# Optimization experiments

Measured on AMD Instinct MI355X. Metric: run time of the kernel, lower is better.

The kernel has to match this reference:

```python
import jax, jax.numpy as jnp
import numpy as np

B, N, D, H = 16, 512, 256, 8
DK = D // H
EPS = 1e-6
NEG_INF = 1e12
LAM_ATT, LAM_DIST, LAM_ADJ = 0.3, 0.3, 0.4


def setup_inputs() -> dict:
    key = jax.random.key(0)
    ks = jax.random.split(key, 16)
    inp = {
        "query": jax.random.normal(ks[0], (B, N, D), jnp.float32),
        "key": jax.random.normal(ks[1], (B, N, D), jnp.float32),
        "value": jax.random.normal(ks[2], (B, N, D), jnp.float32),
        "adj_matrix": jax.random.uniform(ks[3], (B, N, N), jnp.float32),
        "distances_matrix": jax.random.uniform(ks[4], (B, N, N), jnp.float32),
        "edges_att": jnp.zeros((1,), jnp.float32),
        "mask": jnp.ones((B, N), jnp.int32),
    }
    s = 1.0 / np.sqrt(D)
    # four Linear(d_model, d_model): Wq, Wk, Wv, Wo (+ biases)
    for i, nm in enumerate(["q", "k", "v", "o"]):
        inp[f"W{nm}"] = jax.random.normal(ks[5 + 2 * i], (D, D), jnp.float32) * s
        inp[f"b{nm}"] = jax.random.normal(ks[6 + 2 * i], (D,), jnp.float32) * s
    return inp


def _proj(x, W, b):
    # [B,N,D] -> [B,H,N,DK]
    y = x @ W.T + b
    return y.reshape(B, N, H, DK).transpose(0, 2, 1, 3)


def reference(query, key, value, adj_matrix, distances_matrix, edges_att, mask,
              Wq, bq, Wk, bk, Wv, bv, Wo, bo):
    q = _proj(query, Wq, bq)
    k = _proj(key, Wk, bk)
    v = _proj(value, Wv, bv)

    valid = mask != 0  # [B,N] key-side validity

    # distance kernel: softmax(-d) over keys, masked positions -> 0 prob
    d_scores = jnp.where(valid[:, None, :], -distances_matrix, -jnp.inf)
    p_dist = jax.nn.softmax(d_scores, axis=-1)  # [B,N,N]

    # scaled dot-product attention with key mask
    scores = jnp.einsum("bhqd,bhkd->bhqk", q, k) / np.sqrt(DK)
    scores = jnp.where(valid[:, None, None, :], scores, -NEG_INF)
    p_attn = jax.nn.softmax(scores, axis=-1)  # [B,H,N,N]

    # row-normalized adjacency
    p_adj = adj_matrix / (adj_matrix.sum(axis=-1, keepdims=True) + EPS)  # [B,N,N]

    # blend three attention terms (broadcast dist/adj over heads)
    p_weighted = (LAM_ATT * p_attn
                  + LAM_DIST * p_dist[:, None]
                  + LAM_ADJ * p_adj[:, None])  # [B,H,N,N]

    x = jnp.einsum("bhqk,bhkd->bhqd", p_weighted, v)  # [B,H,N,DK]
    x = x.transpose(0, 2, 1, 3).reshape(B, N, D)
    out = x @ Wo.T + bo  # output projection (4th linear)
    return out
```

## Files before the change

kernel.cpp:

```cpp
#include <hip/hip_runtime.h>
#include <cstdint>
#include <cstddef>

#define B_  16
#define N_  512
#define D_  256
#define H_  8
#define DK_ 32

#define QKV_ELEMS 2097152

__device__ __align__(16) unsigned short g_Qb[QKV_ELEMS];
__device__ __align__(16) unsigned short g_Kb[QKV_ELEMS];
__device__ __align__(16) unsigned short g_VT[QKV_ELEMS];
__device__ __align__(16) unsigned short g_WqB[D_*D_];
__device__ __align__(16) unsigned short g_WkB[D_*D_];
__device__ __align__(16) unsigned short g_WvB[D_*D_];
__device__ __align__(16) unsigned short g_WoB[D_*D_];
__device__ __align__(16) unsigned short g_ST[B_*N_*N_];

typedef short v8s __attribute__((ext_vector_type(8)));
typedef float v4f __attribute__((ext_vector_type(4)));

__device__ __forceinline__ unsigned short f2b(float f){
  unsigned int x;
  __builtin_memcpy(&x, &f, 4);
  x = x + 0x7FFFu + ((x >> 16) & 1u);
  return (unsigned short)(x >> 16);
}
__device__ __forceinline__ v8s pack8(const float4 a, const float4 b){
  v8s o;
  o[0]=(short)f2b(a.x); o[1]=(short)f2b(a.y); o[2]=(short)f2b(a.z); o[3]=(short)f2b(a.w);
  o[4]=(short)f2b(b.x); o[5]=(short)f2b(b.y); o[6]=(short)f2b(b.z); o[7]=(short)f2b(b.w);
  return o;
}

__global__ __launch_bounds__(256) void prep_w(
    const float* __restrict__ Wq, const float* __restrict__ Wk,
    const float* __restrict__ Wv, const float* __restrict__ Wo)
{
  const int bid = blockIdx.x;
  const int z = bid >> 6;
  const int i = ((bid & 63)*256 + (int)threadIdx.x)*4;
  const float* src = (z==0)?Wq:(z==1)?Wk:(z==2)?Wv:Wo;
  const float4 u = *reinterpret_cast<const float4*>(src + i);
  ushort4 o4;
  o4.x = f2b(u.x); o4.y = f2b(u.y); o4.z = f2b(u.z); o4.w = f2b(u.w);
  if (z < 3){
    unsigned short* dst = (z==0)?g_WqB:(z==1)?g_WkB:g_WvB;
    *reinterpret_cast<ushort4*>(dst + i) = o4;
  } else {
    const int n = i >> 8, k = i & 255;
    *reinterpret_cast<ushort4*>(g_WoB + ((size_t)(k >> 5))*8192 + (size_t)n*32 + (k & 31)) = o4;
  }
}

__global__ __launch_bounds__(512) void st_kernel(
    const float* __restrict__ dist, const float* __restrict__ adjm,
    const int* __restrict__ mask)
{
  const int bid = blockIdx.x;
  const int b = bid & 15, qt = bid >> 4, q0 = qt*16;
  const int t = threadIdx.x;
  const int row = t >> 5, seg = t & 31;
  const size_t roff = ((size_t)(b*N_ + q0 + row))*N_ + seg*16;
  const float* dp = dist + roff;
  const float* ap = adjm + roff;
  const int*   mp = mask + b*N_ + seg*16;
  const float4 d0 = reinterpret_cast<const float4*>(dp)[0];
  const float4 d1 = reinterpret_cast<const float4*>(dp)[1];
  const float4 d2 = reinterpret_cast<const float4*>(dp)[2];
  const float4 d3 = reinterpret_cast<const float4*>(dp)[3];
  const float4 a0 = reinterpret_cast<const float4*>(ap)[0];
  const float4 a1 = reinterpret_cast<const float4*>(ap)[1];
  const float4 a2 = reinterpret_cast<const float4*>(ap)[2];
  const float4 a3 = reinterpret_cast<const float4*>(ap)[3];
  const int4   m0 = reinterpret_cast<const int4*>(mp)[0];
  const int4   m1 = reinterpret_cast<const int4*>(mp)[1];
  const int4   m2 = reinterpret_cast<const int4*>(mp)[2];
  const int4   m3 = reinterpret_cast<const int4*>(mp)[3];

  float ev[16], av[16];
  #define ST_STEP(i, d4, a4, m4) \
    ev[i+0] = m4.x ? __expf(-d4.x) : 0.f;  av[i+0] = a4.x; \
    ev[i+1] = m4.y ? __expf(-d4.y) : 0.f;  av[i+1] = a4.y; \
    ev[i+2] = m4.z ? __expf(-d4.z) : 0.f;  av[i+2] = a4.z; \
    ev[i+3] = m4.w ? __expf(-d4.w) : 0.f;  av[i+3] = a4.w;
  ST_STEP(0,  d0, a0, m0)
  ST_STEP(4,  d1, a1, m1)
  ST_STEP(8,  d2, a2, m2)
  ST_STEP(12, d3, a3, m3)
  #undef ST_STEP
  float lz = 0.f, la = 0.f;
  #pragma unroll
  for (int i = 0; i < 16; ++i){ lz += ev[i]; la += av[i]; }
  #pragma unroll
  for (int o = 1; o < 32; o <<= 1){
    lz += __shfl_xor(lz, o, 64);
    la += __shfl_xor(la, o, 64);
  }
  const float c0 = (lz > 0.f) ? 0.3f / lz : 0.f;
  const float c1 = 0.4f / (la + 1e-6f);
  v8s s0, s1;
  #pragma unroll
  for (int i = 0; i < 8; ++i){
    s0[i] = (short)f2b(ev[i]*c0   + av[i]*c1);
    s1[i] = (short)f2b(ev[8+i]*c0 + av[8+i]*c1);
  }
  *reinterpret_cast<v8s*>(g_ST + roff)     = s0;
  *reinterpret_cast<v8s*>(g_ST + roff + 8) = s1;
}

__global__ __launch_bounds__(256) void qkv_gemm(
    const float* __restrict__ query, const float* __restrict__ key_,
    const float* __restrict__ value,
    const float* __restrict__ bq, const float* __restrict__ bk,
    const float* __restrict__ bv)
{
  __shared__ unsigned short Wl[64*264];
  const int bid = blockIdx.x;
  const int t   = threadIdx.x;
  const int z  = bid >> 9;
  const int rr = bid & 511;
  const int mt = rr >> 2, nt = rr & 3;
  const float* Ap = (z==0) ? query : (z==1) ? key_ : value;
  const unsigned short* WB = (z==0) ? g_WqB : (z==1) ? g_WkB : g_WvB;
  const float* bp = (z==0) ? bq : (z==1) ? bk : bv;
  const int w = t >> 6, lane = t & 63, kl = lane & 15, quad = lane >> 4;
  const int m0 = mt*64 + w*16;
  const int n0 = nt*64;

  {
    const int row = t >> 2;
    const int ks  = (t & 3) * 64;
    const unsigned short* src = WB + (size_t)(n0+row)*256 + ks;
    unsigned short* dst = Wl + row*264 + ks;
    #pragma unroll
    for (int u = 0; u < 8; ++u)
      *reinterpret_cast<v8s*>(dst + u*8) = *reinterpret_cast<const v8s*>(src + u*8);
  }
  __syncthreads();

  v4f acc[4];
  #pragma unroll
  for (int nb = 0; nb < 4; ++nb) acc[nb] = (v4f){0.f,0.f,0.f,0.f};
  const int arow = m0 + kl;

  if (z == 2){
    #pragma unroll
    for (int k0 = 0; k0 < 256; k0 += 32){
      const float* ap = Ap + (size_t)arow*256 + k0 + quad*8;
      const v8s af = pack8(reinterpret_cast<const float4*>(ap)[0],
                           reinterpret_cast<const float4*>(ap)[1]);
      #pragma unroll
      for (int nb = 0; nb < 4; ++nb){
        const v8s wf = *reinterpret_cast<const v8s*>(&Wl[(nb*16+kl)*264 + k0 + quad*8]);
        acc[nb] = __builtin_amdgcn_mfma_f32_16x16x32_bf16(wf, af, acc[nb], 0, 0, 0);
      }
    }
    const int tok = m0 + kl, bb = tok >> 9, nr = tok & 511;
    #pragma unroll
    for (int nb = 0; nb < 4; ++nb)
      #pragma unroll
      for (int r = 0; r < 4; ++r){
        const int n = n0 + nb*16 + quad*4 + r;
        const float v = acc[nb][r] + bp[n];
        g_VT[(((size_t)bb*H_ + (n>>5))*16 + (nr>>5))*1024 + (size_t)(n&31)*32 + (nr&31)] = f2b(v);
      }
  } else {
    #pragma unroll
    for (int k0 = 0; k0 < 256; k0 += 32){
      const float* ap = Ap + (size_t)arow*256 + k0 + quad*8;
      const v8s af = pack8(reinterpret_cast<const float4*>(ap)[0],
                           reinterpret_cast<const float4*>(ap)[1]);
      #pragma unroll
      for (int nb = 0; nb < 4; ++nb){
        const v8s wf = *reinterpret_cast<const v8s*>(&Wl[(nb*16+kl)*264 + k0 + quad*8]);
        acc[nb] = __builtin_amdgcn_mfma_f32_16x16x32_bf16(af, wf, acc[nb], 0, 0, 0);
      }
    }
    unsigned short* dst = z ? g_Kb : g_Qb;
    #pragma unroll
    for (int nb = 0; nb < 4; ++nb){
      const int n = n0 + nb*16 + kl;
      const float bias = bp[n];
      #pragma unroll
      for (int r = 0; r < 4; ++r){
        const int m = m0 + quad*4 + r;
        const float v = acc[nb][r] + bias;
        dst[(((size_t)(m>>9)*H_ + (n>>5))*N_ + (m&511))*DK_ + (n&31)] = f2b(v);
      }
    }
  }
}

__global__ __launch_bounds__(512, 4) void attn_kernel(
    const int* __restrict__ mask, const float* __restrict__ bo,
    float* __restrict__ out)
{
  __shared__ unsigned short STl[16*520];
  __shared__ unsigned short Pl[8*16*40];
  __shared__ unsigned short Xl[16*272];
  const int bid = blockIdx.x;
  const int b  = bid & 15;
  const int qt = bid >> 4;
  const int q0 = qt*16;
  const int t  = threadIdx.x;
  const int w  = t >> 6, lane = t & 63;
  const int kl = lane & 15, quad = lane >> 4;

  {
    const int row = t >> 5;
    const int c16 = (t & 31) * 16;
    const unsigned short* src = g_ST + ((size_t)(b*N_ + q0 + row))*N_ + c16;
    *reinterpret_cast<v8s*>(&STl[row*520 + c16])     = *reinterpret_cast<const v8s*>(src);
    *reinterpret_cast<v8s*>(&STl[row*520 + c16 + 8]) = *reinterpret_cast<const v8s*>(src + 8);
  }

  const int h = w;
  const size_t bh = (size_t)b*H_ + h;
  const float scale = 0.17677669529663687f;
  const unsigned short* Qp = g_Qb + (bh*N_ + q0)*DK_;
  const unsigned short* Kp = g_Kb + bh*N_*DK_;
  const unsigned short* Vp = g_VT + bh*(size_t)(N_*DK_);
  unsigned short* Plw = Pl + w*640;
  const int* mrow = mask + b*N_;
  const v8s aq = *reinterpret_cast<const v8s*>(Qp + (size_t)kl*DK_ + quad*8);
  const v4f vz = {0.f, 0.f, 0.f, 0.f};

  v4f oA0 = vz, oA1 = vz;
  v4f oS0 = vz, oS1 = vz;
  float lsum[4] = {0.f, 0.f, 0.f, 0.f};

  __syncthreads();

  #pragma unroll 1
  for (int ch = 0; ch < 4; ++ch){
    const int k0 = ch*128;
    v4f acc[8];
    #pragma unroll
    for (int kb = 0; kb < 8; ++kb){
      const v8s bk = *reinterpret_cast<const v8s*>(Kp + (size_t)(k0 + kb*16 + kl)*DK_ + quad*8);
      acc[kb] = __builtin_amdgcn_mfma_f32_16x16x32_bf16(aq, bk, vz, 0, 0, 0);
    }
    #pragma unroll
    for (int kb = 0; kb < 8; ++kb){
      const bool valid = (mrow[k0 + kb*16 + kl] != 0);
      #pragma unroll
      for (int r = 0; r < 4; ++r){
        const float e = valid ? __expf(acc[kb][r]*scale) : 0.f;
        acc[kb][r] = e;
        lsum[r] += e;
      }
    }
    #pragma unroll
    for (int cc = 0; cc < 4; ++cc){
      #pragma unroll
      for (int r = 0; r < 4; ++r){
        Plw[(quad*4 + r)*40 + kl]      = f2b(acc[2*cc    ][r]);
        Plw[(quad*4 + r)*40 + 16 + kl] = f2b(acc[2*cc + 1][r]);
      }
      const int kk = k0 + cc*32;
      const v8s bp  = *reinterpret_cast<const v8s*>(&Plw[kl*40 + quad*8]);
      const v8s bst = *reinterpret_cast<const v8s*>(&STl[kl*520 + kk + quad*8]);
      const v8s av0 = *reinterpret_cast<const v8s*>(Vp + (size_t)(kk + kl)*32 + quad*8);
      const v8s av1 = *reinterpret_cast<const v8s*>(Vp + (size_t)(kk + 16 + kl)*32 + quad*8);
      oA0 = __builtin_amdgcn_mfma_f32_16x16x32_bf16(av0, bp,  oA0, 0, 0, 0);
      oS0 = __builtin_amdgcn_mfma_f32_16x16x32_bf16(av0, bst, oS0, 0, 0, 0);
      oA1 = __builtin_amdgcn_mfma_f32_16x16x32_bf16(av1, bp,  oA1, 0, 0, 0);
      oS1 = __builtin_amdgcn_mfma_f32_16x16x32_bf16(av1, bst, oS1, 0, 0, 0);
    }
  }

  #pragma unroll
  for (int r = 0; r < 4; ++r)
    #pragma unroll
    for (int o = 1; o < 16; o <<= 1) lsum[r] += __shfl_xor(lsum[r], o, 64);
  const float s01 = (kl & 1) ? lsum[1] : lsum[0];
  const float s23 = (kl & 1) ? lsum[3] : lsum[2];
  const float sv  = (kl & 2) ? s23 : s01;
  float inv = __shfl(sv, ((kl >> 2) << 4) | (kl & 3), 64);
  inv = (inv > 0.f) ? 0.3f / inv : 0.f;

  unsigned short* xr = Xl + kl*272 + h*32;
  #pragma unroll
  for (int r = 0; r < 4; ++r){
    xr[     quad*4 + r] = f2b(oA0[r]*inv + oS0[r]);
    xr[16 + quad*4 + r] = f2b(oA1[r]*inv + oS1[r]);
  }
  __syncthreads();

  {
    const int n0 = w*32;
    v4f a2[2];
    a2[0] = vz; a2[1] = vz;
    #pragma unroll
    for (int k0 = 0; k0 < 256; k0 += 32){
      const v8s af = *reinterpret_cast<const v8s*>(&Xl[kl*272 + k0 + quad*8]);
      #pragma unroll
      for (int nb = 0; nb < 2; ++nb){
        const v8s wf = *reinterpret_cast<const v8s*>(
            g_WoB + (size_t)(k0 >> 5)*8192 + (size_t)(n0 + nb*16 + kl)*32 + quad*8);
        a2[nb] = __builtin_amdgcn_mfma_f32_16x16x32_bf16(af, wf, a2[nb], 0, 0, 0);
      }
    }
    #pragma unroll
    for (int nb = 0; nb < 2; ++nb){
      const int n = n0 + nb*16 + kl;
      const float bias = bo[n];
      #pragma unroll
      for (int r = 0; r < 4; ++r)
        out[((size_t)(b*N_ + q0 + quad*4 + r))*256 + n] = a2[nb][r] + bias;
    }
  }
}

extern "C" void kernel_launch(void* const* d_in, const int* in_sizes, int n_in,
                              void* d_out, int out_size, void* d_ws, size_t ws_size,
                              hipStream_t stream)
{
  const float* query = (const float*)d_in[0];
  const float* key_  = (const float*)d_in[1];
  const float* value = (const float*)d_in[2];
  const float* adjm  = (const float*)d_in[3];
  const float* dist  = (const float*)d_in[4];
  const int*   mask  = (const int*)d_in[6];
  const float* Wq = (const float*)d_in[7];  const float* bq = (const float*)d_in[8];
  const float* Wk = (const float*)d_in[9];  const float* bk = (const float*)d_in[10];
  const float* Wv = (const float*)d_in[11]; const float* bv = (const float*)d_in[12];
  const float* Wo = (const float*)d_in[13]; const float* bo = (const float*)d_in[14];

  prep_w<<<256, 256, 0, stream>>>(Wq, Wk, Wv, Wo);
  st_kernel<<<512, 512, 0, stream>>>(dist, adjm, mask);
  qkv_gemm<<<1536, 256, 0, stream>>>(query, key_, value, bq, bk, bv);
  attn_kernel<<<512, 512, 0, stream>>>(mask, bo, (float*)d_out);
}
```

Measured before the change: 165.0 us.

## Merge weight prep into ST kernel and prefetch V/mask before softmax in attention

Weight conversion to bf16 now runs in 32 extra blocks of the ST kernel, removing one launch. In the attention loop, V fragments and mask values for the whole 128-key chunk are loaded up front so their latency overlaps the exp work. All probabilities for the chunk are then written to a wider shared buffer in one pass instead of being interleaved with the PV MFMAs. This raises register and LDS use per block (Pl goes from about 10KB to 35KB), which may cut occupancy below the 4 blocks per CU requested.

```diff
diff --git a/kernel.cpp b/kernel.cpp
--- a/kernel.cpp
+++ b/kernel.cpp
@@ -35,33 +35,39 @@
   return o;
 }
 
-__global__ __launch_bounds__(256) void prep_w(
+__global__ __launch_bounds__(512) void st_prep(
+    const float* __restrict__ dist, const float* __restrict__ adjm,
+    const int* __restrict__ mask,
     const float* __restrict__ Wq, const float* __restrict__ Wk,
     const float* __restrict__ Wv, const float* __restrict__ Wo)
 {
   const int bid = blockIdx.x;
-  const int z = bid >> 6;
-  const int i = ((bid & 63)*256 + (int)threadIdx.x)*4;
-  const float* src = (z==0)?Wq:(z==1)?Wk:(z==2)?Wv:Wo;
-  const float4 u = *reinterpret_cast<const float4*>(src + i);
-  ushort4 o4;
-  o4.x = f2b(u.x); o4.y = f2b(u.y); o4.z = f2b(u.z); o4.w = f2b(u.w);
-  if (z < 3){
-    unsigned short* dst = (z==0)?g_WqB:(z==1)?g_WkB:g_WvB;
-    *reinterpret_cast<ushort4*>(dst + i) = o4;
-  } else {
-    const int n = i >> 8, k = i & 255;
-    *reinterpret_cast<ushort4*>(g_WoB + ((size_t)(k >> 5))*8192 + (size_t)n*32 + (k & 31)) = o4;
-  }
-}
-
-__global__ __launch_bounds__(512) void st_kernel(
-    const float* __restrict__ dist, const float* __restrict__ adjm,
-    const int* __restrict__ mask)
-{
-  const int bid = blockIdx.x;
+  const int t = threadIdx.x;
+
+  if (bid >= 512){
+    const int tid = (bid - 512)*512 + t;
+    #pragma unroll
+    for (int u = 0; u < 4; ++u){
+      const int i4 = tid*4 + u;
+      const int i  = i4*4;
+      const int z  = i >> 16;
+      const int lo = i & 65535;
+      const float* src = (z==0)?Wq:(z==1)?Wk:(z==2)?Wv:Wo;
+      const float4 f = *reinterpret_cast<const float4*>(src + lo);
+      ushort4 o4;
+      o4.x=f2b(f.x); o4.y=f2b(f.y); o4.z=f2b(f.z); o4.w=f2b(f.w);
+      if (z < 3){
+        unsigned short* dst = (z==0)?g_WqB:(z==1)?g_WkB:g_WvB;
+        *reinterpret_cast<ushort4*>(dst + lo) = o4;
+      } else {
+        const int n = lo >> 8, k = lo & 255;
+        *reinterpret_cast<ushort4*>(g_WoB + ((size_t)(k >> 5))*8192 + (size_t)n*32 + (k & 31)) = o4;
+      }
+    }
+    return;
+  }
+
   const int b = bid & 15, qt = bid >> 4, q0 = qt*16;
-  const int t = threadIdx.x;
   const int row = t >> 5, seg = t & 31;
   const size_t roff = ((size_t)(b*N_ + q0 + row))*N_ + seg*16;
   const float* dp = dist + roff;
@@ -199,7 +205,7 @@
     float* __restrict__ out)
 {
   __shared__ unsigned short STl[16*520];
-  __shared__ unsigned short Pl[8*16*40];
+  __shared__ unsigned short Pl[8*16*136];
   __shared__ unsigned short Xl[16*272];
   const int bid = blockIdx.x;
   const int b  = bid & 15;
@@ -223,7 +229,7 @@
   const unsigned short* Qp = g_Qb + (bh*N_ + q0)*DK_;
   const unsigned short* Kp = g_Kb + bh*N_*DK_;
   const unsigned short* Vp = g_VT + bh*(size_t)(N_*DK_);
-  unsigned short* Plw = Pl + w*640;
+  unsigned short* Plw = Pl + w*2176;
   const int* mrow = mask + b*N_;
   const v8s aq = *reinterpret_cast<const v8s*>(Qp + (size_t)kl*DK_ + quad*8);
   const v4f vz = {0.f, 0.f, 0.f, 0.f};
@@ -243,9 +249,19 @@
       const v8s bk = *reinterpret_cast<const v8s*>(Kp + (size_t)(k0 + kb*16 + kl)*DK_ + quad*8);
       acc[kb] = __builtin_amdgcn_mfma_f32_16x16x32_bf16(aq, bk, vz, 0, 0, 0);
     }
+    v8s av[8];
+    int mk[8];
+    #pragma unroll
+    for (int cc = 0; cc < 4; ++cc){
+      const int kk = k0 + cc*32;
+      av[2*cc]   = *reinterpret_cast<const v8s*>(Vp + (size_t)(kk + kl)*32 + quad*8);
+      av[2*cc+1] = *reinterpret_cast<const v8s*>(Vp + (size_t)(kk + 16 + kl)*32 + quad*8);
+    }
+    #pragma unroll
+    for (int kb = 0; kb < 8; ++kb) mk[kb] = mrow[k0 + kb*16 + kl];
     #pragma unroll
     for (int kb = 0; kb < 8; ++kb){
-      const bool valid = (mrow[k0 + kb*16 + kl] != 0);
+      const bool valid = (mk[kb] != 0);
       #pragma unroll
       for (int r = 0; r < 4; ++r){
         const float e = valid ? __expf(acc[kb][r]*scale) : 0.f;
@@ -254,21 +270,19 @@
       }
     }
     #pragma unroll
+    for (int kb = 0; kb < 8; ++kb)
+      #pragma unroll
+      for (int r = 0; r < 4; ++r)
+        Plw[(quad*4 + r)*136 + kb*16 + kl] = f2b(acc[kb][r]);
+    #pragma unroll
     for (int cc = 0; cc < 4; ++cc){
-      #pragma unroll
-      for (int r = 0; r < 4; ++r){
-        Plw[(quad*4 + r)*40 + kl]      = f2b(acc[2*cc    ][r]);
-        Plw[(quad*4 + r)*40 + 16 + kl] = f2b(acc[2*cc + 1][r]);
-      }
       const int kk = k0 + cc*32;
-      const v8s bp  = *reinterpret_cast<const v8s*>(&Plw[kl*40 + quad*8]);
+      const v8s bp  = *reinterpret_cast<const v8s*>(&Plw[kl*136 + cc*32 + quad*8]);
       const v8s bst = *reinterpret_cast<const v8s*>(&STl[kl*520 + kk + quad*8]);
-      const v8s av0 = *reinterpret_cast<const v8s*>(Vp + (size_t)(kk + kl)*32 + quad*8);
-      const v8s av1 = *reinterpret_cast<const v8s*>(Vp + (size_t)(kk + 16 + kl)*32 + quad*8);
-      oA0 = __builtin_amdgcn_mfma_f32_16x16x32_bf16(av0, bp,  oA0, 0, 0, 0);
-      oS0 = __builtin_amdgcn_mfma_f32_16x16x32_bf16(av0, bst, oS0, 0, 0, 0);
-      oA1 = __builtin_amdgcn_mfma_f32_16x16x32_bf16(av1, bp,  oA1, 0, 0, 0);
-      oS1 = __builtin_amdgcn_mfma_f32_16x16x32_bf16(av1, bst, oS1, 0, 0, 0);
+      oA0 = __builtin_amdgcn_mfma_f32_16x16x32_bf16(av[2*cc],   bp,  oA0, 0, 0, 0);
+      oS0 = __builtin_amdgcn_mfma_f32_16x16x32_bf16(av[2*cc],   bst, oS0, 0, 0, 0);
+      oA1 = __builtin_amdgcn_mfma_f32_16x16x32_bf16(av[2*cc+1], bp,  oA1, 0, 0, 0);
+      oS1 = __builtin_amdgcn_mfma_f32_16x16x32_bf16(av[2*cc+1], bst, oS1, 0, 0, 0);
     }
   }
 
@@ -330,8 +344,7 @@
   const float* Wv = (const float*)d_in[11]; const float* bv = (const float*)d_in[12];
   const float* Wo = (const float*)d_in[13]; const float* bo = (const float*)d_in[14];
 
-  prep_w<<<256, 256, 0, stream>>>(Wq, Wk, Wv, Wo);
-  st_kernel<<<512, 512, 0, stream>>>(dist, adjm, mask);
+  st_prep<<<544, 512, 0, stream>>>(dist, adjm, mask, Wq, Wk, Wv, Wo);
   qkv_gemm<<<1536, 256, 0, stream>>>(query, key_, value, bq, bk, bv);
   attn_kernel<<<512, 512, 0, stream>>>(mask, bo, (float*)d_out);
 }
```

Result: no change. 163.7 us (-0.8%).

## Merge ST prep into QKV GEMM launch and keep attention probabilities in registers

Applied to the files above, without the earlier changes.

Combines the distance/adjacency blend kernel with the QKV projection into one launch, with extra blocks handling ST rows, and remaps block indices for the GEMM part. Folds the softmax scale and log2(e) into Q so attention can use exp2 directly. Swaps the MFMA operand order so the scores come out transposed, then passes P to the PV MFMA through packed bf16 converts and cross-lane shuffles instead of an LDS round trip. It also simplifies the row-sum reduction. This removes one launch, the LDS traffic for P and per-element scale multiplies, at the cost of more shuffles and a more fragile lane mapping.

```diff
diff --git a/kernel.cpp b/kernel.cpp
--- a/kernel.cpp
+++ b/kernel.cpp
@@ -21,6 +21,8 @@
 
 typedef short v8s __attribute__((ext_vector_type(8)));
 typedef float v4f __attribute__((ext_vector_type(4)));
+
+#define QSCALE 0.25503485917270874f
 
 __device__ __forceinline__ unsigned short f2b(float f){
   unsigned int x;
@@ -55,71 +57,73 @@
   }
 }
 
-__global__ __launch_bounds__(512) void st_kernel(
+__global__ __launch_bounds__(256) void st_gemm(
+    const float* __restrict__ query, const float* __restrict__ key_,
+    const float* __restrict__ value,
+    const float* __restrict__ bq, const float* __restrict__ bk,
+    const float* __restrict__ bv,
     const float* __restrict__ dist, const float* __restrict__ adjm,
     const int* __restrict__ mask)
 {
-  const int bid = blockIdx.x;
-  const int b = bid & 15, qt = bid >> 4, q0 = qt*16;
-  const int t = threadIdx.x;
-  const int row = t >> 5, seg = t & 31;
-  const size_t roff = ((size_t)(b*N_ + q0 + row))*N_ + seg*16;
-  const float* dp = dist + roff;
-  const float* ap = adjm + roff;
-  const int*   mp = mask + b*N_ + seg*16;
-  const float4 d0 = reinterpret_cast<const float4*>(dp)[0];
-  const float4 d1 = reinterpret_cast<const float4*>(dp)[1];
-  const float4 d2 = reinterpret_cast<const float4*>(dp)[2];
-  const float4 d3 = reinterpret_cast<const float4*>(dp)[3];
-  const float4 a0 = reinterpret_cast<const float4*>(ap)[0];
-  const float4 a1 = reinterpret_cast<const float4*>(ap)[1];
-  const float4 a2 = reinterpret_cast<const float4*>(ap)[2];
-  const float4 a3 = reinterpret_cast<const float4*>(ap)[3];
-  const int4   m0 = reinterpret_cast<const int4*>(mp)[0];
-  const int4   m1 = reinterpret_cast<const int4*>(mp)[1];
-  const int4   m2 = reinterpret_cast<const int4*>(mp)[2];
-  const int4   m3 = reinterpret_cast<const int4*>(mp)[3];
-
-  float ev[16], av[16];
-  #define ST_STEP(i, d4, a4, m4) \
-    ev[i+0] = m4.x ? __expf(-d4.x) : 0.f;  av[i+0] = a4.x; \
-    ev[i+1] = m4.y ? __expf(-d4.y) : 0.f;  av[i+1] = a4.y; \
-    ev[i+2] = m4.z ? __expf(-d4.z) : 0.f;  av[i+2] = a4.z; \
-    ev[i+3] = m4.w ? __expf(-d4.w) : 0.f;  av[i+3] = a4.w;
-  ST_STEP(0,  d0, a0, m0)
-  ST_STEP(4,  d1, a1, m1)
-  ST_STEP(8,  d2, a2, m2)
-  ST_STEP(12, d3, a3, m3)
-  #undef ST_STEP
-  float lz = 0.f, la = 0.f;
-  #pragma unroll
-  for (int i = 0; i < 16; ++i){ lz += ev[i]; la += av[i]; }
-  #pragma unroll
-  for (int o = 1; o < 32; o <<= 1){
-    lz += __shfl_xor(lz, o, 64);
-    la += __shfl_xor(la, o, 64);
-  }
-  const float c0 = (lz > 0.f) ? 0.3f / lz : 0.f;
-  const float c1 = 0.4f / (la + 1e-6f);
-  v8s s0, s1;
-  #pragma unroll
-  for (int i = 0; i < 8; ++i){
-    s0[i] = (short)f2b(ev[i]*c0   + av[i]*c1);
-    s1[i] = (short)f2b(ev[8+i]*c0 + av[8+i]*c1);
-  }
-  *reinterpret_cast<v8s*>(g_ST + roff)     = s0;
-  *reinterpret_cast<v8s*>(g_ST + roff + 8) = s1;
-}
-
-__global__ __launch_bounds__(256) void qkv_gemm(
-    const float* __restrict__ query, const float* __restrict__ key_,
-    const float* __restrict__ value,
-    const float* __restrict__ bq, const float* __restrict__ bk,
-    const float* __restrict__ bv)
-{
   __shared__ unsigned short Wl[64*264];
-  const int bid = blockIdx.x;
-  const int t   = threadIdx.x;
+  const int bid0 = blockIdx.x;
+  const int t    = threadIdx.x;
+
+  if (bid0 >= 1536){
+    const int s = bid0 - 1536;
+    const int b = (s >> 1) & 15, qt = s >> 5, half = s & 1;
+    const int row = half*8 + (t >> 5);
+    const int seg = t & 31;
+    const size_t roff = ((size_t)(b*N_ + qt*16 + row))*N_ + seg*16;
+    const float* dp = dist + roff;
+    const float* ap = adjm + roff;
+    const int*   mp = mask + b*N_ + seg*16;
+    const float4 d0 = reinterpret_cast<const float4*>(dp)[0];
+    const float4 d1 = reinterpret_cast<const float4*>(dp)[1];
+    const float4 d2 = reinterpret_cast<const float4*>(dp)[2];
+    const float4 d3 = reinterpret_cast<const float4*>(dp)[3];
+    const float4 a0 = reinterpret_cast<const float4*>(ap)[0];
+    const float4 a1 = reinterpret_cast<const float4*>(ap)[1];
+    const float4 a2 = reinterpret_cast<const float4*>(ap)[2];
+    const float4 a3 = reinterpret_cast<const float4*>(ap)[3];
+    const int4   m0 = reinterpret_cast<const int4*>(mp)[0];
+    const int4   m1 = reinterpret_cast<const int4*>(mp)[1];
+    const int4   m2 = reinterpret_cast<const int4*>(mp)[2];
+    const int4   m3 = reinterpret_cast<const int4*>(mp)[3];
+
+    float ev[16], av[16];
+    #define ST_STEP(i, d4, a4, m4) \
+      ev[i+0] = m4.x ? __expf(-d4.x) : 0.f;  av[i+0] = a4.x; \
+      ev[i+1] = m4.y ? __expf(-d4.y) : 0.f;  av[i+1] = a4.y; \
+      ev[i+2] = m4.z ? __expf(-d4.z) : 0.f;  av[i+2] = a4.z; \
+      ev[i+3] = m4.w ? __expf(-d4.w) : 0.f;  av[i+3] = a4.w;
+    ST_STEP(0,  d0, a0, m0)
+    ST_STEP(4,  d1, a1, m1)
+    ST_STEP(8,  d2, a2, m2)
+    ST_STEP(12, d3, a3, m3)
+    #undef ST_STEP
+    float lz = 0.f, la = 0.f;
+    #pragma unroll
+    for (int i = 0; i < 16; ++i){ lz += ev[i]; la += av[i]; }
+    #pragma unroll
+    for (int o = 1; o < 32; o <<= 1){
+      lz += __shfl_xor(lz, o, 64);
+      la += __shfl_xor(la, o, 64);
+    }
+    const float c0 = (lz > 0.f) ? 0.3f / lz : 0.f;
+    const float c1 = 0.4f / (la + 1e-6f);
+    v8s s0v, s1v;
+    #pragma unroll
+    for (int i = 0; i < 8; ++i){
+      s0v[i] = (short)f2b(ev[i]*c0   + av[i]*c1);
+      s1v[i] = (short)f2b(ev[8+i]*c0 + av[8+i]*c1);
+    }
+    *reinterpret_cast<v8s*>(g_ST + roff)     = s0v;
+    *reinterpret_cast<v8s*>(g_ST + roff + 8) = s1v;
+    return;
+  }
+
+  const int bid = ((bid0 & 7) * 192) + (bid0 >> 3);
   const int z  = bid >> 9;
   const int rr = bid & 511;
   const int mt = rr >> 2, nt = rr & 3;
@@ -180,6 +184,7 @@
       }
     }
     unsigned short* dst = z ? g_Kb : g_Qb;
+    const float sc = (z == 0) ? QSCALE : 1.0f;
     #pragma unroll
     for (int nb = 0; nb < 4; ++nb){
       const int n = n0 + nb*16 + kl;
@@ -187,7 +192,7 @@
       #pragma unroll
       for (int r = 0; r < 4; ++r){
         const int m = m0 + quad*4 + r;
-        const float v = acc[nb][r] + bias;
+        const float v = (acc[nb][r] + bias) * sc;
         dst[(((size_t)(m>>9)*H_ + (n>>5))*N_ + (m&511))*DK_ + (n&31)] = f2b(v);
       }
     }
@@ -199,7 +204,6 @@
     float* __restrict__ out)
 {
   __shared__ unsigned short STl[16*520];
-  __shared__ unsigned short Pl[8*16*40];
   __shared__ unsigned short Xl[16*272];
   const int bid = blockIdx.x;
   const int b  = bid & 15;
@@ -219,18 +223,20 @@
 
   const int h = w;
   const size_t bh = (size_t)b*H_ + h;
-  const float scale = 0.17677669529663687f;
   const unsigned short* Qp = g_Qb + (bh*N_ + q0)*DK_;
   const unsigned short* Kp = g_Kb + bh*N_*DK_;
   const unsigned short* Vp = g_VT + bh*(size_t)(N_*DK_);
-  unsigned short* Plw = Pl + w*640;
   const int* mrow = mask + b*N_;
   const v8s aq = *reinterpret_cast<const v8s*>(Qp + (size_t)kl*DK_ + quad*8);
   const v4f vz = {0.f, 0.f, 0.f, 0.f};
 
+  const int s0 = ((quad & 1) << 5) + kl;
+  const int s1 = s0 + 16;
+  const int hi = quad >> 1;
+
   v4f oA0 = vz, oA1 = vz;
   v4f oS0 = vz, oS1 = vz;
-  float lsum[4] = {0.f, 0.f, 0.f, 0.f};
+  float lsum = 0.f;
 
   __syncthreads();
 
@@ -241,46 +247,57 @@
     #pragma unroll
     for (int kb = 0; kb < 8; ++kb){
       const v8s bk = *reinterpret_cast<const v8s*>(Kp + (size_t)(k0 + kb*16 + kl)*DK_ + quad*8);
-      acc[kb] = __builtin_amdgcn_mfma_f32_16x16x32_bf16(aq, bk, vz, 0, 0, 0);
+      acc[kb] = __builtin_amdgcn_mfma_f32_16x16x32_bf16(bk, aq, vz, 0, 0, 0);
+    }
+    v8s av[8];
+    #pragma unroll
+    for (int cc = 0; cc < 4; ++cc){
+      const int kk = k0 + cc*32;
+      av[2*cc]   = *reinterpret_cast<const v8s*>(Vp + (size_t)(kk + kl)*32 + quad*8);
+      av[2*cc+1] = *reinterpret_cast<const v8s*>(Vp + (size_t)(kk + 16 + kl)*32 + quad*8);
     }
     #pragma unroll
     for (int kb = 0; kb < 8; ++kb){
-      const bool valid = (mrow[k0 + kb*16 + kl] != 0);
-      #pragma unroll
-      for (int r = 0; r < 4; ++r){
-        const float e = valid ? __expf(acc[kb][r]*scale) : 0.f;
-        acc[kb][r] = e;
-        lsum[r] += e;
-      }
+      const int4 m4 = *reinterpret_cast<const int4*>(mrow + k0 + kb*16 + quad*4);
+      const float e0 = m4.x ? __builtin_amdgcn_exp2f(acc[kb][0]) : 0.f;
+      const float e1 = m4.y ? __builtin_amdgcn_exp2f(acc[kb][1]) : 0.f;
+      const float e2 = m4.z ? __builtin_amdgcn_exp2f(acc[kb][2]) : 0.f;
+      const float e3 = m4.w ? __builtin_amdgcn_exp2f(acc[kb][3]) : 0.f;
+      acc[kb][0]=e0; acc[kb][1]=e1; acc[kb][2]=e2; acc[kb][3]=e3;
+      lsum += e0+e1+e2+e3;
     }
     #pragma unroll
     for (int cc = 0; cc < 4; ++cc){
-      #pragma unroll
-      for (int r = 0; r < 4; ++r){
-        Plw[(quad*4 + r)*40 + kl]      = f2b(acc[2*cc    ][r]);
-        Plw[(quad*4 + r)*40 + 16 + kl] = f2b(acc[2*cc + 1][r]);
-      }
       const int kk = k0 + cc*32;
-      const v8s bp  = *reinterpret_cast<const v8s*>(&Plw[kl*40 + quad*8]);
+      uint32_t pkE0, pkE2, pkO0, pkO2;
+      asm("v_cvt_pk_bf16_f32 %0, %1, %2" : "=v"(pkE0) : "v"(acc[2*cc][0]),   "v"(acc[2*cc][1]));
+      asm("v_cvt_pk_bf16_f32 %0, %1, %2" : "=v"(pkE2) : "v"(acc[2*cc][2]),   "v"(acc[2*cc][3]));
+      asm("v_cvt_pk_bf16_f32 %0, %1, %2" : "=v"(pkO0) : "v"(acc[2*cc+1][0]), "v"(acc[2*cc+1][1]));
+      asm("v_cvt_pk_bf16_f32 %0, %1, %2" : "=v"(pkO2) : "v"(acc[2*cc+1][2]), "v"(acc[2*cc+1][3]));
+      const uint32_t e0a = (uint32_t)__shfl((int)pkE0, s0, 64);
+      const uint32_t o0a = (uint32_t)__shfl((int)pkO0, s0, 64);
+      const uint32_t e2a = (uint32_t)__shfl((int)pkE2, s0, 64);
+      const uint32_t o2a = (uint32_t)__shfl((int)pkO2, s0, 64);
+      const uint32_t e0b = (uint32_t)__shfl((int)pkE0, s1, 64);
+      const uint32_t o0b = (uint32_t)__shfl((int)pkO0, s1, 64);
+      const uint32_t e2b = (uint32_t)__shfl((int)pkE2, s1, 64);
+      const uint32_t o2b = (uint32_t)__shfl((int)pkO2, s1, 64);
+      union { v8s v; uint32_t w4[4]; } bp;
+      bp.w4[0] = hi ? o0a : e0a;
+      bp.w4[1] = hi ? o2a : e2a;
+      bp.w4[2] = hi ? o0b : e0b;
+      bp.w4[3] = hi ? o2b : e2b;
       const v8s bst = *reinterpret_cast<const v8s*>(&STl[kl*520 + kk + quad*8]);
-      const v8s av0 = *reinterpret_cast<const v8s*>(Vp + (size_t)(kk + kl)*32 + quad*8);
-      const v8s av1 = *reinterpret_cast<const v8s*>(Vp + (size_t)(kk + 16 + kl)*32 + quad*8);
-      oA0 = __builtin_amdgcn_mfma_f32_16x16x32_bf16(av0, bp,  oA0, 0, 0, 0);
-      oS0 = __builtin_amdgcn_mfma_f32_16x16x32_bf16(av0, bst, oS0, 0, 0, 0);
-      oA1 = __builtin_amdgcn_mfma_f32_16x16x32_bf16(av1, bp,  oA1, 0, 0, 0);
-      oS1 = __builtin_amdgcn_mfma_f32_16x16x32_bf16(av1, bst, oS1, 0, 0, 0);
-    }
-  }
-
-  #pragma unroll
-  for (int r = 0; r < 4; ++r)
-    #pragma unroll
-    for (int o = 1; o < 16; o <<= 1) lsum[r] += __shfl_xor(lsum[r], o, 64);
-  const float s01 = (kl & 1) ? lsum[1] : lsum[0];
-  const float s23 = (kl & 1) ? lsum[3] : lsum[2];
-  const float sv  = (kl & 2) ? s23 : s01;
-  float inv = __shfl(sv, ((kl >> 2) << 4) | (kl & 3), 64);
-  inv = (inv > 0.f) ? 0.3f / inv : 0.f;
+      oA0 = __builtin_amdgcn_mfma_f32_16x16x32_bf16(av[2*cc],   bp.v, oA0, 0, 0, 0);
+      oS0 = __builtin_amdgcn_mfma_f32_16x16x32_bf16(av[2*cc],   bst,  oS0, 0, 0, 0);
+      oA1 = __builtin_amdgcn_mfma_f32_16x16x32_bf16(av[2*cc+1], bp.v, oA1, 0, 0, 0);
+      oS1 = __builtin_amdgcn_mfma_f32_16x16x32_bf16(av[2*cc+1], bst,  oS1, 0, 0, 0);
+    }
+  }
+
+  lsum += __shfl_xor(lsum, 16, 64);
+  lsum += __shfl_xor(lsum, 32, 64);
+  const float inv = (lsum > 0.f) ? 0.3f / lsum : 0.f;
 
   unsigned short* xr = Xl + kl*272 + h*32;
   #pragma unroll
@@ -331,7 +348,7 @@
   const float* Wo = (const float*)d_in[13]; const float* bo = (const float*)d_in[14];
 
   prep_w<<<256, 256, 0, stream>>>(Wq, Wk, Wv, Wo);
-  st_kernel<<<512, 512, 0, stream>>>(dist, adjm, mask);
-  qkv_gemm<<<1536, 256, 0, stream>>>(query, key_, value, bq, bk, bv);
+  st_gemm<<<2560, 256, 0, stream>>>(query, key_, value, bq, bk, bv,
+                                    dist, adjm, mask);
   attn_kernel<<<512, 512, 0, stream>>>(mask, bo, (float*)d_out);
 }
```

Result: no change. 164.2 us (-0.5%).
